# Kernel tuning notes

Measured on AMD Instinct MI355X. Metric: run time of the kernel, lower is better.

## Reference

```python
import jax, jax.numpy as jnp
import numpy as np

NUM_HEADS = 16


def setup_inputs() -> dict:
    k0 = jax.random.key(0)
    ks = jax.random.split(k0, 5)
    T, S, N, E = 1024, 1024, 8, 1024
    query = jax.random.normal(ks[0], (T, N, E), dtype=jnp.float32)
    key_t = jax.random.normal(ks[1], (S, N, E), dtype=jnp.float32)
    value = jax.random.normal(ks[2], (S, N, E), dtype=jnp.float32)
    # xavier-uniform-like scale for in_proj (fan_in=fan_out-ish): gain*sqrt(6/(3E+E))
    lim_in = float(np.sqrt(6.0 / (3 * E + E)))
    in_proj_weight = jax.random.uniform(ks[3], (3 * E, E), dtype=jnp.float32, minval=-lim_in, maxval=lim_in)
    in_proj_bias = jnp.zeros((3 * E,), dtype=jnp.float32)
    lim_out = float(np.sqrt(1.0 / E))
    out_proj_weight = jax.random.uniform(ks[4], (E, E), dtype=jnp.float32, minval=-lim_out, maxval=lim_out)
    out_proj_bias = jnp.zeros((E,), dtype=jnp.float32)
    return {
        'query': query, 'key': key_t, 'value': value,
        'in_proj_weight': in_proj_weight, 'in_proj_bias': in_proj_bias,
        'out_proj_weight': out_proj_weight, 'out_proj_bias': out_proj_bias,
    }


def reference(query, key, value, in_proj_weight, in_proj_bias, out_proj_weight, out_proj_bias):
    # Faithful to the source: q,k,v ALL come from `query` via the 3E in-projection
    # (the torch code projects only `query` and chunks; key/value tensors unused).
    T, N, E = query.shape
    S = key.shape[0]  # must equal T for the reshape, as in the torch code
    H = NUM_HEADS
    D = E // H
    qkv = jnp.einsum('tne,fe->tnf', query, in_proj_weight) + in_proj_bias  # (T,N,3E)
    q, k, v = jnp.split(qkv, 3, axis=-1)
    q = q * (float(D) ** -0.5)
    # (T, N*H, D) -> (N*H, T, D)
    q = q.reshape(T, N * H, D).transpose(1, 0, 2)
    k = k.reshape(S, N * H, D).transpose(1, 0, 2)
    v = v.reshape(S, N * H, D).transpose(1, 0, 2)
    attn = jnp.einsum('btd,bsd->bts', q, k)          # (N*H, T, S)
    attn = jax.nn.softmax(attn, axis=-1)
    out = jnp.einsum('bts,bsd->btd', attn, v)        # (N*H, T, D)
    out = out.transpose(1, 0, 2).reshape(T, N, E)
    out = jnp.einsum('tne,fe->tnf', out, out_proj_weight) + out_proj_bias
    avg_weights = attn.reshape(N, H, T, S).mean(axis=1)  # (N, T, S)
    return out, avg_weights
```

## Files before the change

kernel.cpp:

```cpp
#include <hip/hip_runtime.h>


typedef __bf16 bf16x8 __attribute__((ext_vector_type(8)));
typedef float f32x4 __attribute__((ext_vector_type(4)));
typedef unsigned int u32;
typedef const __attribute__((address_space(1))) u32 gu32;
typedef __attribute__((address_space(3))) u32 lu32;

#define MFMA(a, b, c) __builtin_amdgcn_mfma_f32_16x16x32_bf16((a), (b), (c), 0, 0, 0)

#if __has_builtin(__builtin_amdgcn_exp2f)
#define EXP2(x) __builtin_amdgcn_exp2f(x)
#else
#define EXP2(x) exp2f(x)
#endif

__device__ __forceinline__ unsigned short f2bf(float x) {
    union { float f; unsigned u; } v; v.f = x;
    unsigned r = v.u + 0x7fffu + ((v.u >> 16) & 1u);
    return (unsigned short)(r >> 16);
}

__device__ __forceinline__ bf16x8 frag_ld(const unsigned short* p) {
    return __builtin_bit_cast(bf16x8, *(const uint4*)p);
}

template<int ROWS>
__device__ __forceinline__ void stageNx64(const unsigned short* g, int gs,
                                          unsigned short* lds, int wave, int lane) {
#pragma unroll
    for (int it = 0; it < ROWS / 32; it++) {
        int chunk = wave * (ROWS / 32) + it;
        int row = chunk * 8 + (lane >> 3);
        int cb = (lane & 7) ^ (row & 7);
        const unsigned short* gp = g + (size_t)row * gs + cb * 8;
        unsigned short* lp = lds + chunk * 512;
        __builtin_amdgcn_global_load_lds((gu32*)gp, (lu32*)lp, 16, 0, 0);
    }
}

__device__ __forceinline__ bf16x8 frag_sw(const unsigned short* lds, int row, int cb) {
    return frag_ld(lds + row * 64 + ((cb ^ (row & 7)) << 3));
}

__global__ void k_convert_all(const float* __restrict__ q, const float* __restrict__ wi,
                              const float* __restrict__ wo,
                              unsigned short* __restrict__ xq, unsigned short* __restrict__ xwi,
                              unsigned short* __restrict__ xwo) {
    int i = blockIdx.x * 256 + threadIdx.x;
    const float* src; unsigned short* dst; int off;
    if (i < 2097152)      { src = q;  dst = xq;  off = i; }
    else if (i < 2883584) { src = wi; dst = xwi; off = i - 2097152; }
    else                  { src = wo; dst = xwo; off = i - 2883584; }
    float4 v = ((const float4*)src)[off];
    ushort4 o;
    o.x = f2bf(v.x); o.y = f2bf(v.y); o.z = f2bf(v.z); o.w = f2bf(v.w);
    ((ushort4*)dst)[off] = o;
}

__global__ __launch_bounds__(256) void k_inproj(
    const unsigned short* __restrict__ A, const unsigned short* __restrict__ B,
    const float* __restrict__ bias,
    unsigned short* __restrict__ qbf, unsigned short* __restrict__ kbf,
    unsigned short* __restrict__ vTbf)
{
    __shared__ unsigned short As[2][128 * 64];
    __shared__ unsigned short Bs[2][128 * 64];
    const int tid = threadIdx.x;
    const int wave = tid >> 6, lane = tid & 63;
    const int quad = lane >> 4, l16 = lane & 15;
    const int wm = wave >> 1, wn = wave & 1;
    const int m0 = blockIdx.x * 128, n0 = blockIdx.y * 128;
    const unsigned short* Ab = A + (size_t)m0 * 1024;
    const unsigned short* Bb = B + (size_t)n0 * 1024;

    f32x4 acc[4][4];
#pragma unroll
    for (int i = 0; i < 4; i++)
#pragma unroll
        for (int j = 0; j < 4; j++) acc[i][j] = (f32x4){0.f, 0.f, 0.f, 0.f};

    stageNx64<128>(Ab, 1024, As[0], wave, lane);
    stageNx64<128>(Bb, 1024, Bs[0], wave, lane);
    __syncthreads();
    for (int it = 0; it < 16; it++) {
        const int cur = it & 1;
        if (it < 15) {
            stageNx64<128>(Ab + (it + 1) * 64, 1024, As[cur ^ 1], wave, lane);
            stageNx64<128>(Bb + (it + 1) * 64, 1024, Bs[cur ^ 1], wave, lane);
        }
#pragma unroll
        for (int kc = 0; kc < 2; kc++) {
            bf16x8 af[4], bfr[4];
#pragma unroll
            for (int i = 0; i < 4; i++) af[i]  = frag_sw(As[cur], wm * 64 + i * 16 + l16, kc * 4 + quad);
#pragma unroll
            for (int j = 0; j < 4; j++) bfr[j] = frag_sw(Bs[cur], wn * 64 + j * 16 + l16, kc * 4 + quad);
#pragma unroll
            for (int i = 0; i < 4; i++)
#pragma unroll
                for (int j = 0; j < 4; j++) acc[i][j] = MFMA(af[i], bfr[j], acc[i][j]);
        }
        __syncthreads();
    }
    const float QSCALE = 0.125f * 1.4426950408889634f;
    const int c = n0 >> 10;
#pragma unroll
    for (int i = 0; i < 4; i++) {
#pragma unroll
        for (int j = 0; j < 4; j++) {
            int col = n0 + wn * 64 + j * 16 + l16;
            float bv = bias[col];
            int hd = col & 1023, h = hd >> 6, d = hd & 63;
#pragma unroll
            for (int r = 0; r < 4; r++) {
                int row = m0 + wm * 64 + i * 16 + quad * 4 + r;
                int t = row >> 3, n = row & 7;
                int b = n * 16 + h;
                float val = acc[i][j][r] + bv;
                if (c == 0)      qbf[(size_t)b * 65536 + t * 64 + d] = f2bf(val * QSCALE);
                else if (c == 1) kbf[(size_t)b * 65536 + t * 64 + d] = f2bf(val);
                else             vTbf[(size_t)b * 65536 + (size_t)d * 1024 + t] = f2bf(val);
            }
        }
    }
}

__global__ __launch_bounds__(256) void k_pv(
    const unsigned short* __restrict__ qbf, const unsigned short* __restrict__ kbf,
    const unsigned short* __restrict__ vTbf,
    float* __restrict__ il_g, unsigned short* __restrict__ Obf)
{
    __shared__ unsigned short Ks[2][64 * 64];
    __shared__ unsigned short Vs[2][64 * 64];
    __shared__ unsigned short Ps[128 * 64];
    const int tid = threadIdx.x;
    const int wave = tid >> 6, lane = tid & 63, quad = lane >> 4, l16 = lane & 15;
    const int blk = blockIdx.x;
    const int xcd = blk & 7, idx = blk >> 3;
    const int b = xcd * 16 + (idx >> 3);
    const int t0 = (idx & 7) * 128;
    const int n = b >> 4, h = b & 15;
    const size_t bb = (size_t)b * 65536;

    bf16x8 aq[2][2];
#pragma unroll
    for (int rf = 0; rf < 2; rf++)
#pragma unroll
        for (int kh = 0; kh < 2; kh++)
            aq[rf][kh] = frag_ld(&qbf[bb + (size_t)(t0 + wave * 32 + rf * 16 + l16) * 64 + kh * 32 + quad * 8]);

    float lsum[2][4];
    f32x4 o[2][4];
#pragma unroll
    for (int rf = 0; rf < 2; rf++)
#pragma unroll
        for (int r = 0; r < 4; r++) lsum[rf][r] = 0.f;
#pragma unroll
    for (int rf = 0; rf < 2; rf++)
#pragma unroll
        for (int df = 0; df < 4; df++) o[rf][df] = (f32x4){0.f, 0.f, 0.f, 0.f};

    stageNx64<64>(kbf + bb, 64, Ks[0], wave, lane);
    stageNx64<64>(vTbf + bb, 1024, Vs[0], wave, lane);
    __syncthreads();
    for (int st = 0; st < 16; st++) {
        const int cur = st & 1;
        if (st < 15) {
            stageNx64<64>(kbf + bb + (size_t)((st + 1) * 64) * 64, 64, Ks[cur ^ 1], wave, lane);
            stageNx64<64>(vTbf + bb + (st + 1) * 64, 1024, Vs[cur ^ 1], wave, lane);
        }
#pragma unroll
        for (int cf = 0; cf < 4; cf++) {
            bf16x8 k0 = frag_sw(Ks[cur], cf * 16 + l16, quad);
            bf16x8 k1 = frag_sw(Ks[cur], cf * 16 + l16, 4 + quad);
#pragma unroll
            for (int rf = 0; rf < 2; rf++) {
                f32x4 z = (f32x4){0.f, 0.f, 0.f, 0.f};
                z = MFMA(aq[rf][0], k0, z);
                z = MFMA(aq[rf][1], k1, z);
#pragma unroll
                for (int r = 0; r < 4; r++) {
                    float p = EXP2(z[r]);
                    lsum[rf][r] += p;
                    int prow = wave * 32 + rf * 16 + quad * 4 + r;
                    int col = cf * 16 + l16;
                    Ps[prow * 64 + (((col >> 3) ^ (prow & 7)) << 3) + (col & 7)] = f2bf(p);
                }
            }
        }
#pragma unroll
        for (int kc = 0; kc < 2; kc++) {
            bf16x8 ap0 = frag_sw(Ps, wave * 32 + l16, kc * 4 + quad);
            bf16x8 ap1 = frag_sw(Ps, wave * 32 + 16 + l16, kc * 4 + quad);
#pragma unroll
            for (int df = 0; df < 4; df++) {
                bf16x8 bv = frag_sw(Vs[cur], df * 16 + l16, kc * 4 + quad);
                o[0][df] = MFMA(ap0, bv, o[0][df]);
                o[1][df] = MFMA(ap1, bv, o[1][df]);
            }
        }
        __syncthreads();
    }
#pragma unroll
    for (int rf = 0; rf < 2; rf++)
#pragma unroll
        for (int r = 0; r < 4; r++) {
            float s = lsum[rf][r];
            s += __shfl_xor(s, 1); s += __shfl_xor(s, 2);
            s += __shfl_xor(s, 4); s += __shfl_xor(s, 8);
            lsum[rf][r] = 1.0f / s;
        }
#pragma unroll
    for (int rf = 0; rf < 2; rf++)
#pragma unroll
        for (int df = 0; df < 4; df++)
#pragma unroll
            for (int r = 0; r < 4; r++) {
                int t = t0 + wave * 32 + rf * 16 + quad * 4 + r;
                Obf[(size_t)(t * 8 + n) * 1024 + h * 64 + df * 16 + l16] = f2bf(o[rf][df][r] * lsum[rf][r]);
            }
    if (l16 == 0) {
#pragma unroll
        for (int rf = 0; rf < 2; rf++)
#pragma unroll
            for (int r = 0; r < 4; r++)
                il_g[(size_t)b * 1024 + t0 + wave * 32 + rf * 16 + quad * 4 + r] = lsum[rf][r];
    }
}

__global__ __launch_bounds__(256) void k_avg(
    const unsigned short* __restrict__ qbf, const unsigned short* __restrict__ kbf,
    const float* __restrict__ il_g, float* __restrict__ avg)
{
    __shared__ unsigned short Qs[2][128 * 64];
    __shared__ unsigned short Ks[2][128 * 64];
    __shared__ float Is[16 * 128];
    const int tid = threadIdx.x;
    const int wave = tid >> 6, lane = tid & 63, quad = lane >> 4, l16 = lane & 15;
    const int wm = wave >> 1, wn = wave & 1;
    const int blk = blockIdx.x;
    const int n = blk & 7, idx = blk >> 3;
    const int s0 = (idx & 7) * 128, t0 = (idx >> 3) * 128;

    for (int i2 = tid; i2 < 2048; i2 += 256)
        Is[i2] = il_g[(size_t)(n * 16 + (i2 >> 7)) * 1024 + t0 + (i2 & 127)];

    f32x4 acc[4][4];
#pragma unroll
    for (int i = 0; i < 4; i++)
#pragma unroll
        for (int j = 0; j < 4; j++) acc[i][j] = (f32x4){0.f, 0.f, 0.f, 0.f};

    stageNx64<128>(qbf + (size_t)(n * 16) * 65536 + (size_t)t0 * 64, 64, Qs[0], wave, lane);
    stageNx64<128>(kbf + (size_t)(n * 16) * 65536 + (size_t)s0 * 64, 64, Ks[0], wave, lane);
    __syncthreads();
    for (int h = 0; h < 16; h++) {
        const int cur = h & 1;
        if (h < 15) {
            const size_t bb1 = (size_t)(n * 16 + h + 1) * 65536;
            stageNx64<128>(qbf + bb1 + (size_t)t0 * 64, 64, Qs[cur ^ 1], wave, lane);
            stageNx64<128>(kbf + bb1 + (size_t)s0 * 64, 64, Ks[cur ^ 1], wave, lane);
        }
        bf16x8 af[4][2];
        float ir[4][4];
#pragma unroll
        for (int i = 0; i < 4; i++) {
            af[i][0] = frag_sw(Qs[cur], wm * 64 + i * 16 + l16, quad);
            af[i][1] = frag_sw(Qs[cur], wm * 64 + i * 16 + l16, 4 + quad);
#pragma unroll
            for (int r = 0; r < 4; r++) ir[i][r] = Is[h * 128 + wm * 64 + i * 16 + quad * 4 + r];
        }
#pragma unroll
        for (int j = 0; j < 4; j++) {
            bf16x8 b0 = frag_sw(Ks[cur], wn * 64 + j * 16 + l16, quad);
            bf16x8 b1 = frag_sw(Ks[cur], wn * 64 + j * 16 + l16, 4 + quad);
#pragma unroll
            for (int i = 0; i < 4; i++) {
                f32x4 z = (f32x4){0.f, 0.f, 0.f, 0.f};
                z = MFMA(af[i][0], b0, z);
                z = MFMA(af[i][1], b1, z);
#pragma unroll
                for (int r = 0; r < 4; r++)
                    acc[i][j][r] += EXP2(z[r]) * ir[i][r];
            }
        }
        __syncthreads();
    }
#pragma unroll
    for (int i = 0; i < 4; i++)
#pragma unroll
        for (int j = 0; j < 4; j++)
#pragma unroll
            for (int r = 0; r < 4; r++) {
                int t = t0 + wm * 64 + i * 16 + quad * 4 + r;
                int s = s0 + wn * 64 + j * 16 + l16;
                avg[(size_t)n * 1048576 + (size_t)t * 1024 + s] = acc[i][j][r] * 0.0625f;
            }
}

__global__ __launch_bounds__(256) void k_outproj(
    const unsigned short* __restrict__ A, const unsigned short* __restrict__ B,
    const float* __restrict__ bias, float* __restrict__ out)
{
    __shared__ unsigned short As[2][128 * 64];
    __shared__ unsigned short Bs[2][128 * 64];
    const int tid = threadIdx.x;
    const int wave = tid >> 6, lane = tid & 63;
    const int quad = lane >> 4, l16 = lane & 15;
    const int wm = wave >> 1, wn = wave & 1;
    const int m0 = blockIdx.x * 128, n0 = blockIdx.y * 128;
    const unsigned short* Ab = A + (size_t)m0 * 1024;
    const unsigned short* Bb = B + (size_t)n0 * 1024;

    f32x4 acc[4][4];
#pragma unroll
    for (int i = 0; i < 4; i++)
#pragma unroll
        for (int j = 0; j < 4; j++) acc[i][j] = (f32x4){0.f, 0.f, 0.f, 0.f};

    stageNx64<128>(Ab, 1024, As[0], wave, lane);
    stageNx64<128>(Bb, 1024, Bs[0], wave, lane);
    __syncthreads();
    for (int it = 0; it < 16; it++) {
        const int cur = it & 1;
        if (it < 15) {
            stageNx64<128>(Ab + (it + 1) * 64, 1024, As[cur ^ 1], wave, lane);
            stageNx64<128>(Bb + (it + 1) * 64, 1024, Bs[cur ^ 1], wave, lane);
        }
#pragma unroll
        for (int kc = 0; kc < 2; kc++) {
            bf16x8 af[4], bfr[4];
#pragma unroll
            for (int i = 0; i < 4; i++) af[i]  = frag_sw(As[cur], wm * 64 + i * 16 + l16, kc * 4 + quad);
#pragma unroll
            for (int j = 0; j < 4; j++) bfr[j] = frag_sw(Bs[cur], wn * 64 + j * 16 + l16, kc * 4 + quad);
#pragma unroll
            for (int i = 0; i < 4; i++)
#pragma unroll
                for (int j = 0; j < 4; j++) acc[i][j] = MFMA(af[i], bfr[j], acc[i][j]);
        }
        __syncthreads();
    }
#pragma unroll
    for (int i = 0; i < 4; i++)
#pragma unroll
        for (int j = 0; j < 4; j++) {
            int col = n0 + wn * 64 + j * 16 + l16;
            float bv = bias[col];
#pragma unroll
            for (int r = 0; r < 4; r++) {
                int row = m0 + wm * 64 + i * 16 + quad * 4 + r;
                out[(size_t)row * 1024 + col] = acc[i][j][r] + bv;
            }
        }
}

extern "C" void kernel_launch(void* const* d_in, const int* in_sizes, int n_in,
                              void* d_out, int out_size, void* d_ws, size_t ws_size,
                              hipStream_t stream)
{
    const float* query = (const float*)d_in[0];
    const float* w_in  = (const float*)d_in[3];
    const float* b_in  = (const float*)d_in[4];
    const float* w_out = (const float*)d_in[5];
    const float* b_out = (const float*)d_in[6];
    float* out = (float*)d_out;
    float* avg = out + 8388608;

    if (ws_size < ((size_t)73 << 20)) return;

    char* ws = (char*)d_ws;
    unsigned short* qbf  = (unsigned short*)(ws);
    unsigned short* kbf  = (unsigned short*)(ws + ((size_t)16 << 20));
    unsigned short* vTbf = (unsigned short*)(ws + ((size_t)32 << 20));
    unsigned short* xbf  = (unsigned short*)(ws + ((size_t)48 << 20));
    unsigned short* wibf = (unsigned short*)(ws + ((size_t)64 << 20));
    unsigned short* wobf = (unsigned short*)(ws + ((size_t)70 << 20));
    float* il_g = (float*)(ws + ((size_t)72 << 20));

    k_convert_all<<<12288, 256, 0, stream>>>(query, w_in, w_out, xbf, wibf, wobf);
    k_inproj<<<dim3(64, 24), 256, 0, stream>>>(xbf, wibf, b_in, qbf, kbf, vTbf);
    k_pv    <<<1024, 256, 0, stream>>>(qbf, kbf, vTbf, il_g, xbf);
    k_avg   <<<512, 256, 0, stream>>>(qbf, kbf, il_g, avg);
    k_outproj<<<dim3(64, 8), 256, 0, stream>>>(xbf, wobf, b_out, out);
}
```

Baseline: 353.8 us.

## Rewrite in-projection GEMM as 256x256 tile, 8-wave ping-pong pipelined kernel

Replaces the 128x128, 4-wave in-projection GEMM with a 256x256 tile, 512-thread kernel using 128KB of dynamic LDS. K-chunk loads are staggered into half-tiles and interleaved with four MFMA phases, using explicit waitcnt, barriers and setprio so global-to-LDS loads overlap compute. The aim is more reuse per byte loaded and hidden memory latency in the largest GEMM. In exchange it needs complex manual synchronization, and the grid drops to 384 blocks, which may underfill the CUs.

```diff
diff --git a/kernel.cpp b/kernel.cpp
--- a/kernel.cpp
+++ b/kernel.cpp
@@ -34,6 +34,19 @@
         int row = chunk * 8 + (lane >> 3);
         int cb = (lane & 7) ^ (row & 7);
         const unsigned short* gp = g + (size_t)row * gs + cb * 8;
+        unsigned short* lp = lds + chunk * 512;
+        __builtin_amdgcn_global_load_lds((gu32*)gp, (lu32*)lp, 16, 0, 0);
+    }
+}
+
+__device__ __forceinline__ void stage_half8(const unsigned short* g,
+                                            unsigned short* lds, int wave, int lane) {
+#pragma unroll
+    for (int it = 0; it < 2; it++) {
+        int chunk = wave * 2 + it;
+        int row = chunk * 8 + (lane >> 3);
+        int cb = (lane & 7) ^ (row & 7);
+        const unsigned short* gp = g + (size_t)row * 1024 + cb * 8;
         unsigned short* lp = lds + chunk * 512;
         __builtin_amdgcn_global_load_lds((gu32*)gp, (lu32*)lp, 16, 0, 0);
     }
@@ -58,55 +71,135 @@
     ((ushort4*)dst)[off] = o;
 }
 
-__global__ __launch_bounds__(256) void k_inproj(
+__global__ __launch_bounds__(512, 2) void k_inproj8(
     const unsigned short* __restrict__ A, const unsigned short* __restrict__ B,
     const float* __restrict__ bias,
     unsigned short* __restrict__ qbf, unsigned short* __restrict__ kbf,
     unsigned short* __restrict__ vTbf)
 {
-    __shared__ unsigned short As[2][128 * 64];
-    __shared__ unsigned short Bs[2][128 * 64];
+    extern __shared__ unsigned short smem[];
+    unsigned short* As = smem;
+    unsigned short* Bs = smem + 32768;
     const int tid = threadIdx.x;
     const int wave = tid >> 6, lane = tid & 63;
     const int quad = lane >> 4, l16 = lane & 15;
-    const int wm = wave >> 1, wn = wave & 1;
-    const int m0 = blockIdx.x * 128, n0 = blockIdx.y * 128;
+    const int wm = wave >> 2, wn = wave & 3;
+    const int m0 = blockIdx.x * 256, n0 = blockIdx.y * 256;
     const unsigned short* Ab = A + (size_t)m0 * 1024;
     const unsigned short* Bb = B + (size_t)n0 * 1024;
 
-    f32x4 acc[4][4];
-#pragma unroll
-    for (int i = 0; i < 4; i++)
+    f32x4 acc[8][4];
+#pragma unroll
+    for (int i = 0; i < 8; i++)
 #pragma unroll
         for (int j = 0; j < 4; j++) acc[i][j] = (f32x4){0.f, 0.f, 0.f, 0.f};
 
-    stageNx64<128>(Ab, 1024, As[0], wave, lane);
-    stageNx64<128>(Bb, 1024, Bs[0], wave, lane);
-    __syncthreads();
-    for (int it = 0; it < 16; it++) {
-        const int cur = it & 1;
-        if (it < 15) {
-            stageNx64<128>(Ab + (it + 1) * 64, 1024, As[cur ^ 1], wave, lane);
-            stageNx64<128>(Bb + (it + 1) * 64, 1024, Bs[cur ^ 1], wave, lane);
-        }
-#pragma unroll
-        for (int kc = 0; kc < 2; kc++) {
-            bf16x8 af[4], bfr[4];
-#pragma unroll
-            for (int i = 0; i < 4; i++) af[i]  = frag_sw(As[cur], wm * 64 + i * 16 + l16, kc * 4 + quad);
-#pragma unroll
-            for (int j = 0; j < 4; j++) bfr[j] = frag_sw(Bs[cur], wn * 64 + j * 16 + l16, kc * 4 + quad);
-#pragma unroll
-            for (int i = 0; i < 4; i++)
-#pragma unroll
-                for (int j = 0; j < 4; j++) acc[i][j] = MFMA(af[i], bfr[j], acc[i][j]);
-        }
-        __syncthreads();
-    }
+    stage_half8(Bb,                  Bs,                 wave, lane);
+    stage_half8(Bb + 128 * 1024,     Bs + 8192,          wave, lane);
+    stage_half8(Ab,                  As,                 wave, lane);
+    stage_half8(Ab + 128 * 1024,     As + 8192,          wave, lane);
+    stage_half8(Bb + 64,             Bs + 16384,         wave, lane);
+    stage_half8(Bb + 128 * 1024 + 64, Bs + 16384 + 8192, wave, lane);
+    asm volatile("s_waitcnt vmcnt(4)" ::: "memory");
+    __builtin_amdgcn_s_barrier();
+
+    bf16x8 a[4][2], b0[2][2], b1[2][2];
+#pragma unroll 2
+    for (int t = 0; t < 16; t++) {
+        unsigned short* Ac = As + (t & 1) * 16384;
+        unsigned short* Bc = Bs + (t & 1) * 16384;
+        const unsigned short* An = Ab + (size_t)(t + 1) * 64;
+        unsigned short* Asn = As + ((t + 1) & 1) * 16384;
+        const unsigned short* Bn = Bb + (size_t)(t + 2) * 64;
+        unsigned short* Bsn = Bs + (t & 1) * 16384;
+
+#pragma unroll
+        for (int i = 0; i < 4; i++)
+#pragma unroll
+            for (int kc = 0; kc < 2; kc++)
+                a[i][kc] = frag_sw(Ac, wm * 128 + i * 16 + l16, kc * 4 + quad);
+#pragma unroll
+        for (int j = 0; j < 2; j++)
+#pragma unroll
+            for (int kc = 0; kc < 2; kc++)
+                b0[j][kc] = frag_sw(Bc, wn * 64 + j * 16 + l16, kc * 4 + quad);
+        if (t < 15) stage_half8(An, Asn, wave, lane);
+        asm volatile("s_waitcnt lgkmcnt(8)" ::: "memory");
+        __builtin_amdgcn_s_barrier();
+        asm volatile("s_waitcnt lgkmcnt(0)" ::: "memory");
+        __builtin_amdgcn_s_setprio(1);
+#pragma unroll
+        for (int i = 0; i < 4; i++)
+#pragma unroll
+            for (int j = 0; j < 2; j++)
+#pragma unroll
+                for (int kc = 0; kc < 2; kc++)
+                    acc[i][j] = MFMA(a[i][kc], b0[j][kc], acc[i][j]);
+        __builtin_amdgcn_s_setprio(0);
+        __builtin_amdgcn_s_barrier();
+
+#pragma unroll
+        for (int j = 0; j < 2; j++)
+#pragma unroll
+            for (int kc = 0; kc < 2; kc++)
+                b1[j][kc] = frag_sw(Bc, wn * 64 + (j + 2) * 16 + l16, kc * 4 + quad);
+        if (t < 15) stage_half8(An + 128 * 1024, Asn + 8192, wave, lane);
+        __builtin_amdgcn_s_barrier();
+        asm volatile("s_waitcnt lgkmcnt(0)" ::: "memory");
+        __builtin_amdgcn_s_setprio(1);
+#pragma unroll
+        for (int i = 0; i < 4; i++)
+#pragma unroll
+            for (int j = 0; j < 2; j++)
+#pragma unroll
+                for (int kc = 0; kc < 2; kc++)
+                    acc[i][j + 2] = MFMA(a[i][kc], b1[j][kc], acc[i][j + 2]);
+        __builtin_amdgcn_s_setprio(0);
+        __builtin_amdgcn_s_barrier();
+
+#pragma unroll
+        for (int i = 0; i < 4; i++)
+#pragma unroll
+            for (int kc = 0; kc < 2; kc++)
+                a[i][kc] = frag_sw(Ac, wm * 128 + (i + 4) * 16 + l16, kc * 4 + quad);
+        if (t < 14) stage_half8(Bn, Bsn, wave, lane);
+        __builtin_amdgcn_s_barrier();
+        asm volatile("s_waitcnt lgkmcnt(0)" ::: "memory");
+        __builtin_amdgcn_s_setprio(1);
+#pragma unroll
+        for (int i = 0; i < 4; i++)
+#pragma unroll
+            for (int j = 0; j < 2; j++)
+#pragma unroll
+                for (int kc = 0; kc < 2; kc++)
+                    acc[i + 4][j + 2] = MFMA(a[i][kc], b1[j][kc], acc[i + 4][j + 2]);
+        __builtin_amdgcn_s_setprio(0);
+        __builtin_amdgcn_s_barrier();
+
+        if (t < 14) stage_half8(Bn + 128 * 1024, Bsn + 8192, wave, lane);
+        __builtin_amdgcn_s_barrier();
+        asm volatile("s_waitcnt lgkmcnt(0)" ::: "memory");
+        __builtin_amdgcn_s_setprio(1);
+#pragma unroll
+        for (int i = 0; i < 4; i++)
+#pragma unroll
+            for (int j = 0; j < 2; j++)
+#pragma unroll
+                for (int kc = 0; kc < 2; kc++)
+                    acc[i + 4][j] = MFMA(a[i][kc], b0[j][kc], acc[i + 4][j]);
+        __builtin_amdgcn_s_setprio(0);
+        if (t < 14) {
+            asm volatile("s_waitcnt vmcnt(4)" ::: "memory");
+        } else if (t == 14) {
+            asm volatile("s_waitcnt vmcnt(0)" ::: "memory");
+        }
+        __builtin_amdgcn_s_barrier();
+    }
+
     const float QSCALE = 0.125f * 1.4426950408889634f;
     const int c = n0 >> 10;
 #pragma unroll
-    for (int i = 0; i < 4; i++) {
+    for (int i = 0; i < 8; i++) {
 #pragma unroll
         for (int j = 0; j < 4; j++) {
             int col = n0 + wn * 64 + j * 16 + l16;
@@ -114,7 +207,7 @@
             int hd = col & 1023, h = hd >> 6, d = hd & 63;
 #pragma unroll
             for (int r = 0; r < 4; r++) {
-                int row = m0 + wm * 64 + i * 16 + quad * 4 + r;
+                int row = m0 + wm * 128 + i * 16 + quad * 4 + r;
                 int t = row >> 3, n = row & 7;
                 int b = n * 16 + h;
                 float val = acc[i][j][r] + bv;
@@ -370,6 +463,13 @@
 
     if (ws_size < ((size_t)73 << 20)) return;
 
+    static bool attr_set = false;
+    if (!attr_set) {
+        (void)hipFuncSetAttribute((const void*)k_inproj8,
+                                  hipFuncAttributeMaxDynamicSharedMemorySize, 131072);
+        attr_set = true;
+    }
+
     char* ws = (char*)d_ws;
     unsigned short* qbf  = (unsigned short*)(ws);
     unsigned short* kbf  = (unsigned short*)(ws + ((size_t)16 << 20));
@@ -380,7 +480,7 @@
     float* il_g = (float*)(ws + ((size_t)72 << 20));
 
     k_convert_all<<<12288, 256, 0, stream>>>(query, w_in, w_out, xbf, wibf, wobf);
-    k_inproj<<<dim3(64, 24), 256, 0, stream>>>(xbf, wibf, b_in, qbf, kbf, vTbf);
+    k_inproj8<<<dim3(32, 12), 512, 131072, stream>>>(xbf, wibf, b_in, qbf, kbf, vTbf);
     k_pv    <<<1024, 256, 0, stream>>>(qbf, kbf, vTbf, il_g, xbf);
     k_avg   <<<512, 256, 0, stream>>>(qbf, kbf, il_g, avg);
     k_outproj<<<dim3(64, 8), 256, 0, stream>>>(xbf, wobf, b_out, out);
```

Measured after the change: 374.1 us. 1.06x slower.
